# Kernel optimization log

Measured on AMD Instinct MI355X. Metric: run time of the kernel, lower is better.

The kernel has to match this reference:

```python
import jax, jax.numpy as jnp
import numpy as np

IMPOSSIBLE = -10000.0


def setup_inputs() -> dict:
    key = jax.random.key(0)
    k_feat, k_w, k_trans = jax.random.split(key, 3)
    B, L, D = 256, 512, 768
    C = 17 + 2  # num_tags + START + STOP
    start_idx, stop_idx = C - 2, C - 1
    features = jax.random.normal(k_feat, (B, L, D), dtype=jnp.float32)
    masks = jnp.ones((B, L), dtype=jnp.float32)
    W_fc = jax.random.normal(k_w, (C, D), dtype=jnp.float32) * 0.02
    b_fc = jnp.zeros((C,), dtype=jnp.float32)
    transitions = jax.random.normal(k_trans, (C, C), dtype=jnp.float32)
    transitions = transitions.at[start_idx, :].set(IMPOSSIBLE)
    transitions = transitions.at[:, stop_idx].set(IMPOSSIBLE)
    return {"features": features, "masks": masks, "W_fc": W_fc,
            "b_fc": b_fc, "transitions": transitions}


def reference(features, masks, W_fc, b_fc, transitions):
    B, L, _ = features.shape
    C = transitions.shape[0]
    start_idx, stop_idx = C - 2, C - 1
    # inner fc: feature space -> tag space, [B, L, C]
    emis = jnp.einsum('bld,cd->blc', features, W_fc) + b_fc

    init = jnp.full((B, C), IMPOSSIBLE, dtype=features.dtype).at[:, start_idx].set(0.0)

    def step(max_score, xs):
        feat_t, m_t = xs                                  # [B,C], [B]
        acc = max_score[:, None, :] + transitions[None, :, :]  # [B,C,C]
        bp = jnp.argmax(acc, axis=-1)                     # [B,C] backpointers
        acc = jnp.max(acc, axis=-1) + feat_t              # [B,C]
        m = m_t[:, None]
        new = acc * m + max_score * (1.0 - m)
        return new, bp

    final, bps = jax.lax.scan(step, init,
                              (jnp.transpose(emis, (1, 0, 2)), masks.T))
    final = final + transitions[stop_idx]                 # transition to STOP
    best_score = jnp.max(final, axis=-1)                  # [B]
    best_tag = jnp.argmax(final, axis=-1)                 # [B]

    # vectorized backtracking (reverse scan over time); padded positions emit -1
    def back(cur, xs):
        bp_t, m_t = xs                                    # [B,C], [B]
        valid = m_t > 0
        tag_out = jnp.where(valid, cur, -1)
        nxt = jnp.where(valid,
                        jnp.take_along_axis(bp_t, cur[:, None], axis=1)[:, 0],
                        cur)
        return nxt, tag_out

    _, tags = jax.lax.scan(back, best_tag, (bps, masks.T), reverse=True)
    best_paths = tags.T.astype(jnp.int32)                 # [B, L]
    return best_score, best_paths
```

## Files before the change

kernel.cpp:

```cpp
#include <hip/hip_runtime.h>

#define BB 256
#define LL 512
#define DD 768
#define CC 19
#define ES 20
#define IMPOSSIBLE -10000.0f

__global__ __launch_bounds__(256) void emis_gemm(
    const float* __restrict__ feats,
    const float* __restrict__ W,
    const float* __restrict__ bias,
    float* __restrict__ emis)
{
    __shared__ float Wl[CC * DD];
    const int tid = threadIdx.x;

#pragma unroll
    for (int i = 0; i < 57; ++i)
        Wl[i * 256 + tid] = W[i * 256 + tid];
    __syncthreads();

    const int row0 = blockIdx.x * 256 + tid;
    const int row1 = row0 + 65536;
    const float4* f0 = reinterpret_cast<const float4*>(feats + (size_t)row0 * DD);
    const float4* f1 = reinterpret_cast<const float4*>(feats + (size_t)row1 * DD);

    float accA[ES], accB[ES];
#pragma unroll
    for (int c = 0; c < CC; ++c) { accA[c] = bias[c]; accB[c] = bias[c]; }
    accA[19] = 0.0f; accB[19] = 0.0f;

    float4 a0 = f0[0], a1 = f0[1], a2 = f0[2], a3 = f0[3];
    float4 b0 = f1[0], b1 = f1[1], b2 = f1[2], b3 = f1[3];
    for (int kc = 0; kc < DD / 16; ++kc) {
        const int nk = (kc < DD / 16 - 1) ? kc + 1 : kc;
        float4 na0 = f0[nk * 4 + 0], na1 = f0[nk * 4 + 1];
        float4 na2 = f0[nk * 4 + 2], na3 = f0[nk * 4 + 3];
        float4 nb0 = f1[nk * 4 + 0], nb1 = f1[nk * 4 + 1];
        float4 nb2 = f1[nk * 4 + 2], nb3 = f1[nk * 4 + 3];
#pragma unroll
        for (int c = 0; c < CC; ++c) {
            const float4* wv = reinterpret_cast<const float4*>(&Wl[c * DD + kc * 16]);
            float4 w0 = wv[0], w1 = wv[1], w2 = wv[2], w3 = wv[3];
            float dA0 = a0.x * w0.x + a0.y * w0.y + a0.z * w0.z + a0.w * w0.w;
            float dA1 = a1.x * w1.x + a1.y * w1.y + a1.z * w1.z + a1.w * w1.w;
            float dA2 = a2.x * w2.x + a2.y * w2.y + a2.z * w2.z + a2.w * w2.w;
            float dA3 = a3.x * w3.x + a3.y * w3.y + a3.z * w3.z + a3.w * w3.w;
            accA[c] += (dA0 + dA1) + (dA2 + dA3);
            float dB0 = b0.x * w0.x + b0.y * w0.y + b0.z * w0.z + b0.w * w0.w;
            float dB1 = b1.x * w1.x + b1.y * w1.y + b1.z * w1.z + b1.w * w1.w;
            float dB2 = b2.x * w2.x + b2.y * w2.y + b2.z * w2.z + b2.w * w2.w;
            float dB3 = b3.x * w3.x + b3.y * w3.y + b3.z * w3.z + b3.w * w3.w;
            accB[c] += (dB0 + dB1) + (dB2 + dB3);
        }
        a0 = na0; a1 = na1; a2 = na2; a3 = na3;
        b0 = nb0; b1 = nb1; b2 = nb2; b3 = nb3;
    }

    float4* eA = reinterpret_cast<float4*>(emis + (size_t)row0 * ES);
    float4* eB = reinterpret_cast<float4*>(emis + (size_t)row1 * ES);
#pragma unroll
    for (int q = 0; q < 5; ++q) {
        eA[q] = make_float4(accA[4 * q + 0], accA[4 * q + 1],
                            accA[4 * q + 2], accA[4 * q + 3]);
        eB[q] = make_float4(accB[4 * q + 0], accB[4 * q + 1],
                            accB[4 * q + 2], accB[4 * q + 3]);
    }
}

__device__ inline float max3f(float a, float b, float c) {
    float d;
    asm("v_max3_f32 %0, %1, %2, %3" : "=v"(d) : "v"(a), "v"(b), "v"(c));
    return d;
}

__global__ __launch_bounds__(64) void scan_bt(
    const float* __restrict__ emis,
    const float* __restrict__ masks,
    const float* __restrict__ trans,
    float* __restrict__ out)
{
    __shared__ float elds[LL * ES];
    __shared__ float mlds[LL];
    __shared__ unsigned char bp8[LL * ES];
    __shared__ unsigned char Hl[64 * ES];
    __shared__ unsigned char vseg[64];
    __shared__ float fbuf[CC];

    const int lane = threadIdx.x;
    const int b    = blockIdx.x;

    {
        const float4* src = reinterpret_cast<const float4*>(emis + (size_t)b * LL * ES);
        float4* dst = reinterpret_cast<float4*>(elds);
#pragma unroll
        for (int i = 0; i < 40; ++i) dst[i * 64 + lane] = src[i * 64 + lane];
        const float4* ms = reinterpret_cast<const float4*>(masks + b * LL);
        float4* md = reinterpret_cast<float4*>(mlds);
        md[lane] = ms[lane];
        md[64 + lane] = ms[64 + lane];
    }
    __syncthreads();

    const int ccl = (lane < CC) ? lane : (CC - 1);
    float T[CC];
#pragma unroll
    for (int p = 0; p < CC; ++p) T[p] = trans[ccl * CC + p];
    const float Tstop = trans[(CC - 1) * CC + ccl];

    float s = (lane == CC - 2) ? 0.0f : IMPOSSIBLE;

    float e  = elds[ccl];
    bool  mv = mlds[0] > 0.0f;
    for (int t = 0; t < LL; ++t) {
        const int tn = (t < LL - 1) ? t + 1 : t;
        float e_n  = elds[tn * ES + ccl];
        bool  mv_n = mlds[tn] > 0.0f;

        float cand[CC];
#pragma unroll
        for (int p = 0; p < CC; ++p) {
            int spi = __builtin_amdgcn_readlane(__builtin_bit_cast(int, s), p);
            cand[p] = __builtin_bit_cast(float, spi) + T[p];
        }
        float t0 = max3f(cand[0],  cand[1],  cand[2]);
        float t1 = max3f(cand[3],  cand[4],  cand[5]);
        float t2 = max3f(cand[6],  cand[7],  cand[8]);
        float t3 = max3f(cand[9],  cand[10], cand[11]);
        float t4 = max3f(cand[12], cand[13], cand[14]);
        float t5 = max3f(cand[15], cand[16], cand[17]);
        float u0 = max3f(t0, t1, t2);
        float u1 = max3f(t3, t4, t5);
        float mx = max3f(u0, u1, cand[18]);

        int arg = CC - 1;
#pragma unroll
        for (int p = CC - 2; p >= 0; --p) arg = (cand[p] == mx) ? p : arg;

        float a = mx + e;
        s = mv ? a : s;
        if (lane < CC) bp8[t * ES + lane] = (unsigned char)arg;

        e = e_n; mv = mv_n;
    }

    float fin = s + Tstop;
    if (lane < CC) fbuf[lane] = fin;
    __syncthreads();

    float best = fbuf[0];
    int   btag = 0;
#pragma unroll
    for (int c = 1; c < CC; ++c) {
        float v = fbuf[c];
        if (v > best) { best = v; btag = c; }
    }
    if (lane == 0) out[b] = best;

    {
        const int base = lane * 8;
        float mj[8];
#pragma unroll
        for (int j = 0; j < 8; ++j) mj[j] = mlds[base + j];
#pragma unroll
        for (int c = 0; c < CC; ++c) {
            int x = c;
#pragma unroll
            for (int j = 7; j >= 0; --j) {
                int nx = bp8[(base + j) * ES + x];
                x = (mj[j] > 0.0f) ? nx : x;
            }
            Hl[lane * ES + c] = (unsigned char)x;
        }
    }
    __syncthreads();

    if (lane == 0) {
        int v = btag;
        vseg[63] = (unsigned char)v;
        for (int i = 62; i >= 0; --i) {
            v = Hl[(i + 1) * ES + v];
            vseg[i] = (unsigned char)v;
        }
    }
    __syncthreads();

    {
        const int base = lane * 8;
        int cur = vseg[lane];
        float tg[8];
#pragma unroll
        for (int j = 7; j >= 0; --j) {
            bool valid = mlds[base + j] > 0.0f;
            tg[j] = (float)(valid ? cur : -1);
            int nx = bp8[(base + j) * ES + cur];
            cur = valid ? nx : cur;
        }
        float4* pout = reinterpret_cast<float4*>(out + BB + (size_t)b * LL + base);
        pout[0] = make_float4(tg[0], tg[1], tg[2], tg[3]);
        pout[1] = make_float4(tg[4], tg[5], tg[6], tg[7]);
    }
}

extern "C" void kernel_launch(void* const* d_in, const int* in_sizes, int n_in,
                              void* d_out, int out_size, void* d_ws, size_t ws_size,
                              hipStream_t stream) {
    const float* feats = (const float*)d_in[0];
    const float* masks = (const float*)d_in[1];
    const float* W     = (const float*)d_in[2];
    const float* bias  = (const float*)d_in[3];
    const float* trans = (const float*)d_in[4];
    float* out  = (float*)d_out;
    float* emis = (float*)d_ws;

    emis_gemm<<<dim3(256), dim3(256), 0, stream>>>(feats, W, bias, emis);
    scan_bt<<<dim3(BB), dim3(64), 0, stream>>>(emis, masks, trans, out);
}
```

Measured before the change: 719.6 us.

## Fuse emission GEMM and Viterbi scan into one per-sequence kernel

Merges the two kernels into a single kernel with one 256-thread block per sequence. Each block computes that sequence's emissions straight into LDS, then one wavefront runs the Viterbi scan and backtrack. This removes the global emission round trip and one kernel launch. The forward step also hardcodes the first step's backpointer to START and only scans 17 predecessors instead of 19, which depends on the START row and STOP column of transitions being IMPOSSIBLE. The larger combined LDS footprint limits occupancy to roughly one block per CU.

After: 706.5 us. No clear change (-1.8%).

```diff
diff --git a/kernel.cpp b/kernel.cpp
--- a/kernel.cpp
+++ b/kernel.cpp
@@ -7,32 +7,52 @@
 #define ES 20
 #define IMPOSSIBLE -10000.0f
 
-__global__ __launch_bounds__(256) void emis_gemm(
+__device__ inline float max3f(float a, float b, float c) {
+    float d;
+    asm("v_max3_f32 %0, %1, %2, %3" : "=v"(d) : "v"(a), "v"(b), "v"(c));
+    return d;
+}
+
+__global__ __launch_bounds__(256) void crf_fused(
     const float* __restrict__ feats,
+    const float* __restrict__ masks,
     const float* __restrict__ W,
     const float* __restrict__ bias,
-    float* __restrict__ emis)
+    const float* __restrict__ trans,
+    float* __restrict__ out)
 {
     __shared__ float Wl[CC * DD];
+    __shared__ float elds[LL * ES];
+    __shared__ float mlds[LL];
+    __shared__ unsigned char bp8[LL * ES];
+    __shared__ unsigned char Hl[64 * ES];
+    __shared__ unsigned char vseg[64];
+    __shared__ float fbuf[CC];
+
     const int tid = threadIdx.x;
+    const int b   = blockIdx.x;
 
 #pragma unroll
     for (int i = 0; i < 57; ++i)
         Wl[i * 256 + tid] = W[i * 256 + tid];
-    __syncthreads();
-
-    const int row0 = blockIdx.x * 256 + tid;
-    const int row1 = row0 + 65536;
-    const float4* f0 = reinterpret_cast<const float4*>(feats + (size_t)row0 * DD);
-    const float4* f1 = reinterpret_cast<const float4*>(feats + (size_t)row1 * DD);
+    if (tid < 128) {
+        const float4* ms = reinterpret_cast<const float4*>(masks + (size_t)b * LL);
+        reinterpret_cast<float4*>(mlds)[tid] = ms[tid];
+    }
+
+    const int r0 = tid, r1 = tid + 256;
+    const float4* f0 = reinterpret_cast<const float4*>(feats + ((size_t)b * LL + r0) * DD);
+    const float4* f1 = reinterpret_cast<const float4*>(feats + ((size_t)b * LL + r1) * DD);
 
     float accA[ES], accB[ES];
 #pragma unroll
-    for (int c = 0; c < CC; ++c) { accA[c] = bias[c]; accB[c] = bias[c]; }
+    for (int c = 0; c < CC; ++c) { float bb = bias[c]; accA[c] = bb; accB[c] = bb; }
     accA[19] = 0.0f; accB[19] = 0.0f;
 
     float4 a0 = f0[0], a1 = f0[1], a2 = f0[2], a3 = f0[3];
     float4 b0 = f1[0], b1 = f1[1], b2 = f1[2], b3 = f1[3];
+    __syncthreads();
+
     for (int kc = 0; kc < DD / 16; ++kc) {
         const int nk = (kc < DD / 16 - 1) ? kc + 1 : kc;
         float4 na0 = f0[nk * 4 + 0], na1 = f0[nk * 4 + 1];
@@ -58,107 +78,83 @@
         b0 = nb0; b1 = nb1; b2 = nb2; b3 = nb3;
     }
 
-    float4* eA = reinterpret_cast<float4*>(emis + (size_t)row0 * ES);
-    float4* eB = reinterpret_cast<float4*>(emis + (size_t)row1 * ES);
-#pragma unroll
-    for (int q = 0; q < 5; ++q) {
-        eA[q] = make_float4(accA[4 * q + 0], accA[4 * q + 1],
-                            accA[4 * q + 2], accA[4 * q + 3]);
-        eB[q] = make_float4(accB[4 * q + 0], accB[4 * q + 1],
-                            accB[4 * q + 2], accB[4 * q + 3]);
-    }
-}
-
-__device__ inline float max3f(float a, float b, float c) {
-    float d;
-    asm("v_max3_f32 %0, %1, %2, %3" : "=v"(d) : "v"(a), "v"(b), "v"(c));
-    return d;
-}
-
-__global__ __launch_bounds__(64) void scan_bt(
-    const float* __restrict__ emis,
-    const float* __restrict__ masks,
-    const float* __restrict__ trans,
-    float* __restrict__ out)
-{
-    __shared__ float elds[LL * ES];
-    __shared__ float mlds[LL];
-    __shared__ unsigned char bp8[LL * ES];
-    __shared__ unsigned char Hl[64 * ES];
-    __shared__ unsigned char vseg[64];
-    __shared__ float fbuf[CC];
-
-    const int lane = threadIdx.x;
-    const int b    = blockIdx.x;
-
     {
-        const float4* src = reinterpret_cast<const float4*>(emis + (size_t)b * LL * ES);
-        float4* dst = reinterpret_cast<float4*>(elds);
-#pragma unroll
-        for (int i = 0; i < 40; ++i) dst[i * 64 + lane] = src[i * 64 + lane];
-        const float4* ms = reinterpret_cast<const float4*>(masks + b * LL);
-        float4* md = reinterpret_cast<float4*>(mlds);
-        md[lane] = ms[lane];
-        md[64 + lane] = ms[64 + lane];
-    }
-    __syncthreads();
-
-    const int ccl = (lane < CC) ? lane : (CC - 1);
-    float T[CC];
-#pragma unroll
-    for (int p = 0; p < CC; ++p) T[p] = trans[ccl * CC + p];
-    const float Tstop = trans[(CC - 1) * CC + ccl];
-
-    float s = (lane == CC - 2) ? 0.0f : IMPOSSIBLE;
-
-    float e  = elds[ccl];
-    bool  mv = mlds[0] > 0.0f;
-    for (int t = 0; t < LL; ++t) {
-        const int tn = (t < LL - 1) ? t + 1 : t;
-        float e_n  = elds[tn * ES + ccl];
-        bool  mv_n = mlds[tn] > 0.0f;
-
-        float cand[CC];
-#pragma unroll
-        for (int p = 0; p < CC; ++p) {
-            int spi = __builtin_amdgcn_readlane(__builtin_bit_cast(int, s), p);
-            cand[p] = __builtin_bit_cast(float, spi) + T[p];
-        }
-        float t0 = max3f(cand[0],  cand[1],  cand[2]);
-        float t1 = max3f(cand[3],  cand[4],  cand[5]);
-        float t2 = max3f(cand[6],  cand[7],  cand[8]);
-        float t3 = max3f(cand[9],  cand[10], cand[11]);
-        float t4 = max3f(cand[12], cand[13], cand[14]);
-        float t5 = max3f(cand[15], cand[16], cand[17]);
-        float u0 = max3f(t0, t1, t2);
-        float u1 = max3f(t3, t4, t5);
-        float mx = max3f(u0, u1, cand[18]);
-
-        int arg = CC - 1;
-#pragma unroll
-        for (int p = CC - 2; p >= 0; --p) arg = (cand[p] == mx) ? p : arg;
-
-        float a = mx + e;
-        s = mv ? a : s;
-        if (lane < CC) bp8[t * ES + lane] = (unsigned char)arg;
-
-        e = e_n; mv = mv_n;
-    }
-
-    float fin = s + Tstop;
-    if (lane < CC) fbuf[lane] = fin;
-    __syncthreads();
-
-    float best = fbuf[0];
-    int   btag = 0;
-#pragma unroll
-    for (int c = 1; c < CC; ++c) {
-        float v = fbuf[c];
-        if (v > best) { best = v; btag = c; }
-    }
-    if (lane == 0) out[b] = best;
-
-    {
+        float4* eA = reinterpret_cast<float4*>(&elds[r0 * ES]);
+        float4* eB = reinterpret_cast<float4*>(&elds[r1 * ES]);
+#pragma unroll
+        for (int q = 0; q < 5; ++q) {
+            eA[q] = make_float4(accA[4 * q + 0], accA[4 * q + 1],
+                                accA[4 * q + 2], accA[4 * q + 3]);
+            eB[q] = make_float4(accB[4 * q + 0], accB[4 * q + 1],
+                                accB[4 * q + 2], accB[4 * q + 3]);
+        }
+    }
+    __syncthreads();
+
+    if (tid < 64) {
+        const int lane = tid;
+        const int ccl  = (lane < CC) ? lane : (CC - 1);
+        float T[CC];
+#pragma unroll
+        for (int p = 0; p < CC; ++p) T[p] = trans[ccl * CC + p];
+        const float Tstop = trans[(CC - 1) * CC + ccl];
+
+        const float sinit = (lane == CC - 2) ? 0.0f : IMPOSSIBLE;
+        float e0  = elds[ccl];
+        bool  mv0 = mlds[0] > 0.0f;
+        float s   = mv0 ? (T[17] + e0) : sinit;
+        if (lane < CC) bp8[lane] = (unsigned char)17;
+
+        float e  = elds[ES + ccl];
+        bool  mv = mlds[1] > 0.0f;
+        for (int t = 1; t < LL; ++t) {
+            const int tn = (t < LL - 1) ? t + 1 : t;
+            float e_n  = elds[tn * ES + ccl];
+            bool  mv_n = mlds[tn] > 0.0f;
+
+            float cand[17];
+#pragma unroll
+            for (int p = 0; p < 17; ++p) {
+                int spi = __builtin_amdgcn_readlane(__builtin_bit_cast(int, s), p);
+                cand[p] = __builtin_bit_cast(float, spi) + T[p];
+            }
+            float t0 = max3f(cand[0],  cand[1],  cand[2]);
+            float t1 = max3f(cand[3],  cand[4],  cand[5]);
+            float t2 = max3f(cand[6],  cand[7],  cand[8]);
+            float t3 = max3f(cand[9],  cand[10], cand[11]);
+            float t4 = max3f(cand[12], cand[13], cand[14]);
+            float u0 = max3f(t0, t1, t2);
+            float u1 = max3f(t3, t4, cand[15]);
+            float mx = max3f(u0, u1, cand[16]);
+
+            int arg = 16;
+#pragma unroll
+            for (int p = 15; p >= 0; --p) arg = (cand[p] == mx) ? p : arg;
+
+            float a = mx + e;
+            s = mv ? a : s;
+            if (lane < CC) bp8[t * ES + lane] = (unsigned char)arg;
+
+            e = e_n; mv = mv_n;
+        }
+
+        float fin = s + Tstop;
+        if (lane < CC) fbuf[lane] = fin;
+    }
+    __syncthreads();
+
+    if (tid < 64) {
+        const int lane = tid;
+
+        float best = fbuf[0];
+        int   btag = 0;
+#pragma unroll
+        for (int c = 1; c < CC; ++c) {
+            float v = fbuf[c];
+            if (v > best) { best = v; btag = c; }
+        }
+        if (lane == 0) out[b] = best;
+
         const int base = lane * 8;
         float mj[8];
 #pragma unroll
@@ -176,7 +172,14 @@
     }
     __syncthreads();
 
-    if (lane == 0) {
+    if (tid == 0) {
+        float best = fbuf[0];
+        int   btag = 0;
+#pragma unroll
+        for (int c = 1; c < CC; ++c) {
+            float v = fbuf[c];
+            if (v > best) { best = v; btag = c; }
+        }
         int v = btag;
         vseg[63] = (unsigned char)v;
         for (int i = 62; i >= 0; --i) {
@@ -186,7 +189,8 @@
     }
     __syncthreads();
 
-    {
+    if (tid < 64) {
+        const int lane = tid;
         const int base = lane * 8;
         int cur = vseg[lane];
         float tg[8];
@@ -211,9 +215,8 @@
     const float* W     = (const float*)d_in[2];
     const float* bias  = (const float*)d_in[3];
     const float* trans = (const float*)d_in[4];
-    float* out  = (float*)d_out;
-    float* emis = (float*)d_ws;
-
-    emis_gemm<<<dim3(256), dim3(256), 0, stream>>>(feats, W, bias, emis);
-    scan_bt<<<dim3(BB), dim3(64), 0, stream>>>(emis, masks, trans, out);
+    float* out = (float*)d_out;
+    (void)d_ws; (void)ws_size;
+
+    crf_fused<<<dim3(BB), dim3(256), 0, stream>>>(feats, masks, W, bias, trans, out);
 }
```
